# Kernel optimization log

Measured on AMD Instinct MI355X. Metric: run time of the kernel, lower is better.

The kernel has to match this reference:

```python
import jax, jax.numpy as jnp
import numpy as np

N_TOKENS = 4096
NUM_IN = 512
OUTPUT_DIMS = [512, 512, 256]
TOTAL_OUT = sum(OUTPUT_DIMS)  # 1280
N_EXPERTS = 8
TOP_K = 2
TEBD_DIM = 64
NTYPES = 128


def setup_inputs() -> dict:
    key = jax.random.key(0)
    ks = jax.random.split(key, 6)
    x = jax.random.normal(ks[0], (N_TOKENS, NUM_IN), dtype=jnp.float32)
    type_embeddings = jax.random.normal(ks[1], (NTYPES, TEBD_DIM), dtype=jnp.float32)
    atom_types = jax.random.randint(ks[2], (N_TOKENS,), 0, NTYPES)
    # learned parameters
    gate_in_dim = NUM_IN + TEBD_DIM
    W_gate = jax.random.normal(ks[3], (gate_in_dim, N_EXPERTS), dtype=jnp.float32) / np.sqrt(gate_in_dim)
    W_exp = jax.random.normal(ks[4], (N_EXPERTS, NUM_IN, TOTAL_OUT), dtype=jnp.float32) / np.sqrt(NUM_IN)
    b_exp = jax.random.normal(ks[5], (N_EXPERTS, TOTAL_OUT), dtype=jnp.float32) * 0.01
    return {"x": x, "type_embeddings": type_embeddings, "atom_types": atom_types,
            "W_gate": W_gate, "W_exp": W_exp, "b_exp": b_exp}


def reference(x, type_embeddings, atom_types, W_gate, W_exp, b_exp):
    # --- gating: atom-type-conditioned router (tebd_dim > 0) ---
    tebd = type_embeddings[atom_types]                      # [N, T]
    gate_in = jnp.concatenate([x, tebd], axis=-1)           # [N, D+T]
    logits = gate_in @ W_gate                               # [N, E]
    top_v, top_i = jax.lax.top_k(logits, TOP_K)             # [N, k]
    probs = jax.nn.softmax(top_v, axis=-1)                  # renormalized over selected experts
    # dense sparse-gate matrix [N, E] (zeros for unselected experts)
    gates = jnp.sum(jax.nn.one_hot(top_i, N_EXPERTS, dtype=x.dtype) * probs[..., None], axis=1)
    # --- expert compute (grouped GEMM expressed densely) ---
    y_all = jnp.einsum('nd,edo->neo', x, W_exp) + b_exp     # [N, E, O]
    fused = jnp.einsum('ne,neo->no', gates, y_all)          # [N, TOTAL_OUT]
    # --- split fused output per head ---
    splits = np.cumsum(OUTPUT_DIMS)[:-1].tolist()
    return tuple(jnp.split(fused, splits, axis=-1))
```

## Files before the change

kernel.cpp:

```cpp
#include <hip/hip_runtime.h>
#include <hip/hip_bf16.h>
#include <cstdint>
#include <cmath>

#define NT 4096
#define DIN 512
#define DOUT 1280
#define NE 8
#define TDIM 64
#define MAXTILES 80
#define NB 10
#define GATE_BLOCKS (NT / 4)
#define CONVW_BLOCKS (20 * (DIN / 64) * NE)
#define S1ROWS 5120

typedef __attribute__((ext_vector_type(8))) short bhalf8;
typedef __attribute__((ext_vector_type(8))) unsigned short ushort8;
typedef __attribute__((ext_vector_type(4))) float f32x4;

__device__ __forceinline__ unsigned short f2bf(float f) {
    __hip_bfloat16 h = __float2bfloat16(f);
    return *reinterpret_cast<unsigned short*>(&h);
}
__device__ __forceinline__ float bf2f(unsigned short u) {
    unsigned int v = (unsigned int)u << 16;
    return *reinterpret_cast<float*>(&v);
}

__device__ __forceinline__ void glds16(const unsigned short* g, unsigned short* l) {
    __builtin_amdgcn_global_load_lds(
        (const __attribute__((address_space(1))) void*)g,
        (__attribute__((address_space(3))) void*)l, 16, 0, 0);
}

__global__ __launch_bounds__(256) void prep_kernel(
    const float* __restrict__ x, const float* __restrict__ temb,
    const int* __restrict__ atype, const float* __restrict__ Wg,
    const float* __restrict__ W,
    unsigned short* __restrict__ xb, unsigned short* __restrict__ WT,
    int* __restrict__ e0a, int* __restrict__ e1a,
    float* __restrict__ g0a, float* __restrict__ g1a)
{
    __shared__ unsigned short t[64 * 72];
    const int tid = threadIdx.x;

    if ((int)blockIdx.x < GATE_BLOCKS) {
        const int n = blockIdx.x * 4 + (tid >> 6);
        const int l = tid & 63;

        float acc[NE];
#pragma unroll
        for (int e = 0; e < NE; ++e) acc[e] = 0.f;

        const float* xr = x + (size_t)n * DIN;
#pragma unroll
        for (int i = 0; i < DIN / 64; ++i) {
            const int k = i * 64 + l;
            const float xv = xr[k];
            xb[(size_t)n * DIN + k] = f2bf(xv);
            const float* wr = Wg + (size_t)k * NE;
#pragma unroll
            for (int e = 0; e < NE; ++e) acc[e] = fmaf(xv, wr[e], acc[e]);
        }
        {
            const int tt = atype[n];
            const float tv = temb[(size_t)tt * TDIM + l];
            const float* wr = Wg + (size_t)(DIN + l) * NE;
#pragma unroll
            for (int e = 0; e < NE; ++e) acc[e] = fmaf(tv, wr[e], acc[e]);
        }
#pragma unroll
        for (int off = 32; off > 0; off >>= 1) {
#pragma unroll
            for (int e = 0; e < NE; ++e) acc[e] += __shfl_xor(acc[e], off, 64);
        }
        if (l == 0) {
            int e0 = 0; float v0 = acc[0];
#pragma unroll
            for (int e = 1; e < NE; ++e) if (acc[e] > v0) { v0 = acc[e]; e0 = e; }
            int e1 = -1; float v1 = -INFINITY;
#pragma unroll
            for (int e = 0; e < NE; ++e) {
                if (e == e0) continue;
                if (acc[e] > v1) { v1 = acc[e]; e1 = e; }
            }
            const float p1 = expf(v1 - v0);
            const float s  = 1.f + p1;
            e0a[n] = e0; e1a[n] = e1; g0a[n] = 1.f / s; g1a[n] = p1 / s;
        }
    } else {
        const int b  = blockIdx.x - GATE_BLOCKS;
        const int n0 = (b % 20) * 64;
        const int k0 = ((b / 20) % (DIN / 64)) * 64;
        const int e  = b / (20 * (DIN / 64));
        const int nl = tid & 63;
        const int kb = tid >> 6;
#pragma unroll
        for (int r = 0; r < 16; ++r) {
            const int kl = r * 4 + kb;
            t[nl * 72 + kl] = f2bf(W[((size_t)e * DIN + k0 + kl) * DOUT + n0 + nl]);
        }
        __syncthreads();
        const int nw = tid >> 2;
        const int kc = tid & 3;
        uint4* dst = reinterpret_cast<uint4*>(
            WT + ((size_t)e * DOUT + n0 + nw) * DIN + k0 + kc * 16);
        const uint4* src = reinterpret_cast<const uint4*>(&t[nw * 72 + kc * 16]);
        dst[0] = src[0];
        dst[1] = src[1];
    }
}

#define SORT_T 1024
__global__ __launch_bounds__(1024) void sort_kernel(
    const int* __restrict__ e0a, const int* __restrict__ e1a,
    const float* __restrict__ g0a, const float* __restrict__ g1a,
    int* __restrict__ perm, float* __restrict__ pgate,
    int* __restrict__ tile_group, int* __restrict__ ipos1,
    int* __restrict__ meta2)
{
    __shared__ int hist[16 * SORT_T];
    __shared__ int gtot[16], gbase[16];
    const int t = threadIdx.x;
    for (int i = t; i < MAXTILES * 128; i += SORT_T) { perm[i] = 0; pgate[i] = 0.f; }
#pragma unroll
    for (int g = 0; g < 16; ++g) hist[g * SORT_T + t] = 0;
    __syncthreads();

    const int nbase = t * 4;
    int keys[8];
#pragma unroll
    for (int i = 0; i < 4; ++i) {
        const int n = nbase + i;
        keys[2 * i]     = e0a[n];
        keys[2 * i + 1] = 8 + e1a[n];
    }
#pragma unroll
    for (int i = 0; i < 8; ++i) hist[keys[i] * SORT_T + t] += 1;
    __syncthreads();

    const int w = t >> 6, l = t & 63;
    {
        int running = 0;
        for (int c = 0; c < SORT_T / 64; ++c) {
            int v = hist[w * SORT_T + c * 64 + l];
            int inc = v;
#pragma unroll
            for (int d = 1; d < 64; d <<= 1) {
                int u = __shfl_up(inc, d, 64);
                if (l >= d) inc += u;
            }
            hist[w * SORT_T + c * 64 + l] = running + inc - v;
            running += __shfl(inc, 63, 64);
        }
        if (l == 0) gtot[w] = running;
    }
    __syncthreads();
    if (t == 0) {
        int s = 0;
#pragma unroll
        for (int g = 0; g < 16; ++g) {
            gbase[g] = s;
            const int ntg = (gtot[g] + 127) >> 7;
            for (int k = 0; k < ntg; ++k) tile_group[s / 128 + k] = g;
            s += ntg * 128;
        }
        meta2[0] = s / 128;
        meta2[1] = gbase[8];
    }
    __syncthreads();

#pragma unroll
    for (int i = 0; i < 4; ++i) {
        const int n = nbase + i;
        {
            const int k = keys[2 * i];
            const int pos = gbase[k] + hist[k * SORT_T + t]++;
            perm[pos] = n; pgate[pos] = g0a[n];
        }
        {
            const int k = keys[2 * i + 1];
            const int pos = gbase[k] + hist[k * SORT_T + t]++;
            perm[pos] = n; pgate[pos] = g1a[n];
            ipos1[n] = pos - gbase[8];
        }
    }
}

__device__ __forceinline__ int swz(int row, int chunk) {
    return row * 64 + ((chunk ^ (row & 7)) << 3);
}

__global__ __launch_bounds__(256, 4) void gemm_kernel(
    const unsigned short* __restrict__ Xb,
    const unsigned short* __restrict__ WT,
    const float* __restrict__ bexp,
    const int* __restrict__ perm, const float* __restrict__ pgate,
    const int* __restrict__ tile_group, const int* __restrict__ meta2,
    unsigned short* __restrict__ stage, float* __restrict__ out)
{
    constexpr int NWG = MAXTILES * NB, CPX = NWG / 8;
    const int gid = blockIdx.x;
    const int wid = (gid & 7) * CPX + (gid >> 3);
    const int tile = wid / NB, nb = wid % NB;
    if (tile >= meta2[0]) return;
    const int g  = tile_group[tile];
    const int e  = g & 7;
    const bool s1 = (g >= 8);
    const int n0 = nb * 128;
    const int ph = tile & 7;

    __shared__ unsigned short As[128 * 64];
    __shared__ unsigned short Bs[128 * 64];
    __shared__ int   toks[128];
    __shared__ float gts[128];

    const int tid = threadIdx.x;
    if (tid < 128) {
        toks[tid] = perm[tile * 128 + tid];
        gts[tid]  = pgate[tile * 128 + tid];
    }
    __syncthreads();

    const int l = tid & 63;
    const int w = tid >> 6;
    const int lrow = l >> 3;
    const int schk = (l & 7) ^ lrow;

    const unsigned short* asrc[4];
    unsigned short* aldsb[4];
#pragma unroll
    for (int i = 0; i < 4; ++i) {
        asrc[i]  = Xb + (size_t)toks[i * 32 + w * 8 + lrow] * DIN + schk * 8;
        aldsb[i] = &As[(i * 32 + w * 8) * 64];
    }
    const unsigned short* bsrc[4];
    unsigned short* bldsb[4];
#pragma unroll
    for (int j = 0; j < 4; ++j) {
        bsrc[j]  = WT + ((size_t)e * DOUT + n0 + j * 32 + w * 8 + lrow) * DIN + schk * 8;
        bldsb[j] = &Bs[(j * 32 + w * 8) * 64];
    }

    f32x4 acc[4][4];
#pragma unroll
    for (int a = 0; a < 4; ++a)
#pragma unroll
        for (int b = 0; b < 4; ++b) acc[a][b] = (f32x4){0.f, 0.f, 0.f, 0.f};

    const int wm = w >> 1, wn = w & 1;
    const int fr = l & 15;
    const int fh = l >> 4;

#pragma unroll
    for (int t = 0; t < DIN / 64; ++t) {
        const int k0 = (((t + ph) & 7)) * 64;
        __syncthreads();
#pragma unroll
        for (int i = 0; i < 4; ++i) glds16(asrc[i] + k0, aldsb[i]);
#pragma unroll
        for (int j = 0; j < 4; ++j) glds16(bsrc[j] + k0, bldsb[j]);
        __syncthreads();
#pragma unroll
        for (int ks = 0; ks < 2; ++ks) {
            bhalf8 af[4], bff[4];
#pragma unroll
            for (int fm = 0; fm < 4; ++fm)
                af[fm] = *reinterpret_cast<const bhalf8*>(
                    &As[swz(wm * 64 + fm * 16 + fr, ks * 4 + fh)]);
#pragma unroll
            for (int fn = 0; fn < 4; ++fn)
                bff[fn] = *reinterpret_cast<const bhalf8*>(
                    &Bs[swz(wn * 64 + fn * 16 + fr, ks * 4 + fh)]);
#pragma unroll
            for (int fm = 0; fm < 4; ++fm)
#pragma unroll
                for (int fn = 0; fn < 4; ++fn)
                    acc[fm][fn] = __builtin_amdgcn_mfma_f32_16x16x32_bf16(
                        af[fm], bff[fn], acc[fm][fn], 0, 0, 0);
        }
    }

    const int lc = l & 15, lr = l >> 4;
    float bval[4];
#pragma unroll
    for (int fn = 0; fn < 4; ++fn)
        bval[fn] = bexp[(size_t)e * DOUT + n0 + wn * 64 + fn * 16 + lc];

    if (s1) {
        const int srow0 = tile * 128 - meta2[1];
#pragma unroll
        for (int fm = 0; fm < 4; ++fm) {
#pragma unroll
            for (int j = 0; j < 4; ++j) {
                const int row = wm * 64 + fm * 16 + lr * 4 + j;
                const float gg = gts[row];
                unsigned short* sp = stage + (size_t)(srow0 + row) * DOUT + n0 + wn * 64 + lc;
#pragma unroll
                for (int fn = 0; fn < 4; ++fn)
                    sp[fn * 16] = f2bf(gg * (acc[fm][fn][j] + bval[fn]));
            }
        }
    } else {
        size_t base; int width, cstart;
        if (n0 < 512)       { base = 0;                 width = 512; cstart = n0; }
        else if (n0 < 1024) { base = (size_t)NT * 512;  width = 512; cstart = n0 - 512; }
        else                { base = (size_t)NT * 1024; width = 256; cstart = n0 - 1024; }
        const int coloff = cstart + wn * 64 + lc;
#pragma unroll
        for (int fm = 0; fm < 4; ++fm) {
#pragma unroll
            for (int j = 0; j < 4; ++j) {
                const int row = wm * 64 + fm * 16 + lr * 4 + j;
                const float gg = gts[row];
                if (gg != 0.f) {
                    float* op = out + base + (size_t)toks[row] * width + coloff;
#pragma unroll
                    for (int fn = 0; fn < 4; ++fn)
                        op[fn * 16] = gg * (acc[fm][fn][j] + bval[fn]);
                }
            }
        }
    }
}

__global__ __launch_bounds__(256) void combine_kernel(
    const unsigned short* __restrict__ stage, const int* __restrict__ ipos1,
    float* __restrict__ out)
{
    const int n = blockIdx.x * 4 + (threadIdx.x >> 6);
    const int l = threadIdx.x & 63;
    const ushort8* srow = reinterpret_cast<const ushort8*>(
        stage + (size_t)ipos1[n] * DOUT);
#pragma unroll
    for (int c = l; c < DOUT / 8; c += 64) {
        const ushort8 v8 = srow[c];
        const int col0 = c * 8;
        float* p;
        if (col0 < 512)       p = out + (size_t)n * 512 + col0;
        else if (col0 < 1024) p = out + (size_t)NT * 512 + (size_t)n * 512 + (col0 - 512);
        else                  p = out + (size_t)NT * 1024 + (size_t)n * 256 + (col0 - 1024);
        f32x4* pv = reinterpret_cast<f32x4*>(p);
        f32x4 a0 = pv[0], a1 = pv[1];
#pragma unroll
        for (int j = 0; j < 4; ++j) a0[j] += bf2f(v8[j]);
#pragma unroll
        for (int j = 0; j < 4; ++j) a1[j] += bf2f(v8[4 + j]);
        pv[0] = a0; pv[1] = a1;
    }
}

extern "C" void kernel_launch(void* const* d_in, const int* in_sizes, int n_in,
                              void* d_out, int out_size, void* d_ws, size_t ws_size,
                              hipStream_t stream) {
    const float* x     = (const float*)d_in[0];
    const float* temb  = (const float*)d_in[1];
    const int*   atype = (const int*)d_in[2];
    const float* Wg    = (const float*)d_in[3];
    const float* Wexp  = (const float*)d_in[4];
    const float* bexp  = (const float*)d_in[5];
    float* out = (float*)d_out;
    char*  ws  = (char*)d_ws;

    unsigned short* xb = (unsigned short*)(ws);
    unsigned short* wt = (unsigned short*)(ws + (size_t)4194304);
    unsigned short* stage = (unsigned short*)(ws + (size_t)14680064);
    const size_t META = 14680064 + (size_t)S1ROWS * DOUT * 2;
    char* meta = ws + META;
    int*   e0a = (int*)(meta);
    int*   e1a = (int*)(meta + 16384);
    float* g0a = (float*)(meta + 32768);
    float* g1a = (float*)(meta + 49152);
    int*   perm       = (int*)(meta + 65536);
    float* pgate      = (float*)(meta + 106496);
    int*   tile_group = (int*)(meta + 147456);
    int*   ipos1      = (int*)(meta + 147968);
    int*   meta2      = (int*)(meta + 164352);

    prep_kernel<<<dim3(GATE_BLOCKS + CONVW_BLOCKS), dim3(256), 0, stream>>>(
        x, temb, atype, Wg, Wexp, xb, wt, e0a, e1a, g0a, g1a);
    sort_kernel<<<dim3(1), dim3(SORT_T), 0, stream>>>(
        e0a, e1a, g0a, g1a, perm, pgate, tile_group, ipos1, meta2);
    gemm_kernel<<<dim3(MAXTILES * NB), dim3(256), 0, stream>>>(
        xb, wt, bexp, perm, pgate, tile_group, meta2, stage, out);
    combine_kernel<<<dim3(NT / 4), dim3(256), 0, stream>>>(stage, ipos1, out);
}
```

Before: 61.40 us.

## Overlap routing sort with weight conversion; vectorize gate x loads

The weight bf16 transpose-conversion moves out of the gating kernel and into a new kernel whose block 0 does the expert sort (now 256 threads, 16 tokens each), while the other 1280 blocks convert weights. The single-block sort therefore overlaps the weight conversion instead of running alone serially. The gating kernel now loads x as 8 contiguous floats per lane and writes bf16 as one 16-byte store. Risks: block 0 has a long serial sort that may become the tail of the mixed kernel, and the smaller sort block has less parallelism.

```diff
diff --git a/kernel.cpp b/kernel.cpp
--- a/kernel.cpp
+++ b/kernel.cpp
@@ -10,8 +10,6 @@
 #define TDIM 64
 #define MAXTILES 80
 #define NB 10
-#define GATE_BLOCKS (NT / 4)
-#define CONVW_BLOCKS (20 * (DIN / 64) * NE)
 #define S1ROWS 5120
 
 typedef __attribute__((ext_vector_type(8))) short bhalf8;
@@ -33,157 +31,158 @@
         (__attribute__((address_space(3))) void*)l, 16, 0, 0);
 }
 
-__global__ __launch_bounds__(256) void prep_kernel(
+__global__ __launch_bounds__(256) void gate_kernel(
     const float* __restrict__ x, const float* __restrict__ temb,
     const int* __restrict__ atype, const float* __restrict__ Wg,
-    const float* __restrict__ W,
-    unsigned short* __restrict__ xb, unsigned short* __restrict__ WT,
+    unsigned short* __restrict__ xb,
     int* __restrict__ e0a, int* __restrict__ e1a,
     float* __restrict__ g0a, float* __restrict__ g1a)
 {
-    __shared__ unsigned short t[64 * 72];
-    const int tid = threadIdx.x;
-
-    if ((int)blockIdx.x < GATE_BLOCKS) {
-        const int n = blockIdx.x * 4 + (tid >> 6);
-        const int l = tid & 63;
-
-        float acc[NE];
-#pragma unroll
-        for (int e = 0; e < NE; ++e) acc[e] = 0.f;
-
-        const float* xr = x + (size_t)n * DIN;
-#pragma unroll
-        for (int i = 0; i < DIN / 64; ++i) {
-            const int k = i * 64 + l;
-            const float xv = xr[k];
-            xb[(size_t)n * DIN + k] = f2bf(xv);
-            const float* wr = Wg + (size_t)k * NE;
-#pragma unroll
-            for (int e = 0; e < NE; ++e) acc[e] = fmaf(xv, wr[e], acc[e]);
-        }
-        {
-            const int tt = atype[n];
-            const float tv = temb[(size_t)tt * TDIM + l];
-            const float* wr = Wg + (size_t)(DIN + l) * NE;
-#pragma unroll
-            for (int e = 0; e < NE; ++e) acc[e] = fmaf(tv, wr[e], acc[e]);
-        }
-#pragma unroll
-        for (int off = 32; off > 0; off >>= 1) {
-#pragma unroll
-            for (int e = 0; e < NE; ++e) acc[e] += __shfl_xor(acc[e], off, 64);
-        }
-        if (l == 0) {
-            int e0 = 0; float v0 = acc[0];
-#pragma unroll
-            for (int e = 1; e < NE; ++e) if (acc[e] > v0) { v0 = acc[e]; e0 = e; }
-            int e1 = -1; float v1 = -INFINITY;
-#pragma unroll
-            for (int e = 0; e < NE; ++e) {
-                if (e == e0) continue;
-                if (acc[e] > v1) { v1 = acc[e]; e1 = e; }
-            }
-            const float p1 = expf(v1 - v0);
-            const float s  = 1.f + p1;
-            e0a[n] = e0; e1a[n] = e1; g0a[n] = 1.f / s; g1a[n] = p1 / s;
-        }
-    } else {
-        const int b  = blockIdx.x - GATE_BLOCKS;
-        const int n0 = (b % 20) * 64;
-        const int k0 = ((b / 20) % (DIN / 64)) * 64;
-        const int e  = b / (20 * (DIN / 64));
-        const int nl = tid & 63;
-        const int kb = tid >> 6;
-#pragma unroll
-        for (int r = 0; r < 16; ++r) {
-            const int kl = r * 4 + kb;
-            t[nl * 72 + kl] = f2bf(W[((size_t)e * DIN + k0 + kl) * DOUT + n0 + nl]);
-        }
-        __syncthreads();
-        const int nw = tid >> 2;
-        const int kc = tid & 3;
-        uint4* dst = reinterpret_cast<uint4*>(
-            WT + ((size_t)e * DOUT + n0 + nw) * DIN + k0 + kc * 16);
-        const uint4* src = reinterpret_cast<const uint4*>(&t[nw * 72 + kc * 16]);
-        dst[0] = src[0];
-        dst[1] = src[1];
-    }
-}
-
-#define SORT_T 1024
-__global__ __launch_bounds__(1024) void sort_kernel(
+    const int n = blockIdx.x * 4 + (threadIdx.x >> 6);
+    const int l = threadIdx.x & 63;
+
+    float acc[NE];
+#pragma unroll
+    for (int e = 0; e < NE; ++e) acc[e] = 0.f;
+
+    const f32x4* xr = reinterpret_cast<const f32x4*>(x + (size_t)n * DIN);
+    const f32x4 v0 = xr[l * 2], v1 = xr[l * 2 + 1];
+    float xv[8] = {v0[0], v0[1], v0[2], v0[3], v1[0], v1[1], v1[2], v1[3]};
+    ushort8 xo;
+#pragma unroll
+    for (int j = 0; j < 8; ++j) xo[j] = f2bf(xv[j]);
+    *reinterpret_cast<ushort8*>(xb + (size_t)n * DIN + l * 8) = xo;
+#pragma unroll
+    for (int j = 0; j < 8; ++j) {
+        const float* wr = Wg + (size_t)(l * 8 + j) * NE;
+#pragma unroll
+        for (int e = 0; e < NE; ++e) acc[e] = fmaf(xv[j], wr[e], acc[e]);
+    }
+    {
+        const int tt = atype[n];
+        const float tv = temb[(size_t)tt * TDIM + l];
+        const float* wr = Wg + (size_t)(DIN + l) * NE;
+#pragma unroll
+        for (int e = 0; e < NE; ++e) acc[e] = fmaf(tv, wr[e], acc[e]);
+    }
+#pragma unroll
+    for (int off = 32; off > 0; off >>= 1) {
+#pragma unroll
+        for (int e = 0; e < NE; ++e) acc[e] += __shfl_xor(acc[e], off, 64);
+    }
+    if (l == 0) {
+        int e0 = 0; float v = acc[0];
+#pragma unroll
+        for (int e = 1; e < NE; ++e) if (acc[e] > v) { v = acc[e]; e0 = e; }
+        int e1 = -1; float v1m = -INFINITY;
+#pragma unroll
+        for (int e = 0; e < NE; ++e) {
+            if (e == e0) continue;
+            if (acc[e] > v1m) { v1m = acc[e]; e1 = e; }
+        }
+        const float p1 = expf(v1m - v);
+        const float s  = 1.f + p1;
+        e0a[n] = e0; e1a[n] = e1; g0a[n] = 1.f / s; g1a[n] = p1 / s;
+    }
+}
+
+#define ST 256
+__global__ __launch_bounds__(256) void mix_kernel(
+    const float* __restrict__ W, unsigned short* __restrict__ WT,
     const int* __restrict__ e0a, const int* __restrict__ e1a,
     const float* __restrict__ g0a, const float* __restrict__ g1a,
     int* __restrict__ perm, float* __restrict__ pgate,
     int* __restrict__ tile_group, int* __restrict__ ipos1,
     int* __restrict__ meta2)
 {
-    __shared__ int hist[16 * SORT_T];
+    __shared__ int hist[16 * ST];
     __shared__ int gtot[16], gbase[16];
+    __shared__ unsigned short tbuf[64 * 72];
     const int t = threadIdx.x;
-    for (int i = t; i < MAXTILES * 128; i += SORT_T) { perm[i] = 0; pgate[i] = 0.f; }
-#pragma unroll
-    for (int g = 0; g < 16; ++g) hist[g * SORT_T + t] = 0;
-    __syncthreads();
-
-    const int nbase = t * 4;
-    int keys[8];
-#pragma unroll
-    for (int i = 0; i < 4; ++i) {
-        const int n = nbase + i;
-        keys[2 * i]     = e0a[n];
-        keys[2 * i + 1] = 8 + e1a[n];
-    }
-#pragma unroll
-    for (int i = 0; i < 8; ++i) hist[keys[i] * SORT_T + t] += 1;
-    __syncthreads();
-
-    const int w = t >> 6, l = t & 63;
-    {
-        int running = 0;
-        for (int c = 0; c < SORT_T / 64; ++c) {
-            int v = hist[w * SORT_T + c * 64 + l];
-            int inc = v;
-#pragma unroll
-            for (int d = 1; d < 64; d <<= 1) {
-                int u = __shfl_up(inc, d, 64);
-                if (l >= d) inc += u;
-            }
-            hist[w * SORT_T + c * 64 + l] = running + inc - v;
-            running += __shfl(inc, 63, 64);
-        }
-        if (l == 0) gtot[w] = running;
-    }
-    __syncthreads();
-    if (t == 0) {
-        int s = 0;
-#pragma unroll
-        for (int g = 0; g < 16; ++g) {
-            gbase[g] = s;
-            const int ntg = (gtot[g] + 127) >> 7;
-            for (int k = 0; k < ntg; ++k) tile_group[s / 128 + k] = g;
-            s += ntg * 128;
-        }
-        meta2[0] = s / 128;
-        meta2[1] = gbase[8];
-    }
-    __syncthreads();
-
-#pragma unroll
-    for (int i = 0; i < 4; ++i) {
-        const int n = nbase + i;
-        {
-            const int k = keys[2 * i];
-            const int pos = gbase[k] + hist[k * SORT_T + t]++;
-            perm[pos] = n; pgate[pos] = g0a[n];
-        }
-        {
-            const int k = keys[2 * i + 1];
-            const int pos = gbase[k] + hist[k * SORT_T + t]++;
-            perm[pos] = n; pgate[pos] = g1a[n];
-            ipos1[n] = pos - gbase[8];
-        }
+
+    if (blockIdx.x == 0) {
+        for (int i = t; i < MAXTILES * 128; i += ST) { perm[i] = 0; pgate[i] = 0.f; }
+#pragma unroll
+        for (int g = 0; g < 16; ++g) hist[g * ST + t] = 0;
+        __syncthreads();
+
+#pragma unroll
+        for (int i = 0; i < 16; ++i) {
+            const int n = t * 16 + i;
+            hist[e0a[n] * ST + t] += 1;
+            hist[(8 + e1a[n]) * ST + t] += 1;
+        }
+        __syncthreads();
+
+        const int w = t >> 6, l = t & 63;
+#pragma unroll
+        for (int q = 0; q < 4; ++q) {
+            const int g = w * 4 + q;
+            int running = 0;
+#pragma unroll
+            for (int c = 0; c < ST / 64; ++c) {
+                int v = hist[g * ST + c * 64 + l];
+                int inc = v;
+#pragma unroll
+                for (int d = 1; d < 64; d <<= 1) {
+                    int u = __shfl_up(inc, d, 64);
+                    if (l >= d) inc += u;
+                }
+                hist[g * ST + c * 64 + l] = running + inc - v;
+                running += __shfl(inc, 63, 64);
+            }
+            if (l == 0) gtot[g] = running;
+        }
+        __syncthreads();
+        if (t == 0) {
+            int s = 0;
+#pragma unroll
+            for (int g = 0; g < 16; ++g) {
+                gbase[g] = s;
+                const int ntg = (gtot[g] + 127) >> 7;
+                for (int k = 0; k < ntg; ++k) tile_group[s / 128 + k] = g;
+                s += ntg * 128;
+            }
+            meta2[0] = s / 128;
+            meta2[1] = gbase[8];
+        }
+        __syncthreads();
+
+#pragma unroll
+        for (int i = 0; i < 16; ++i) {
+            const int n = t * 16 + i;
+            {
+                const int k = e0a[n];
+                const int pos = gbase[k] + hist[k * ST + t]++;
+                perm[pos] = n; pgate[pos] = g0a[n];
+            }
+            {
+                const int k = 8 + e1a[n];
+                const int pos = gbase[k] + hist[k * ST + t]++;
+                perm[pos] = n; pgate[pos] = g1a[n];
+                ipos1[n] = pos - gbase[8];
+            }
+        }
+    } else {
+        const int b  = blockIdx.x - 1;
+        const int n0 = (b % 20) * 64;
+        const int k0 = ((b / 20) % (DIN / 64)) * 64;
+        const int e  = b / (20 * (DIN / 64));
+        const int nl = t & 63;
+        const int kb = t >> 6;
+#pragma unroll
+        for (int r = 0; r < 16; ++r) {
+            const int kl = r * 4 + kb;
+            tbuf[nl * 72 + kl] = f2bf(W[((size_t)e * DIN + k0 + kl) * DOUT + n0 + nl]);
+        }
+        __syncthreads();
+        const int nw = t >> 2;
+        const int kc = t & 3;
+        uint4* dst = reinterpret_cast<uint4*>(
+            WT + ((size_t)e * DOUT + n0 + nw) * DIN + k0 + kc * 16);
+        const uint4* src = reinterpret_cast<const uint4*>(&tbuf[nw * 72 + kc * 16]);
+        dst[0] = src[0];
+        dst[1] = src[1];
     }
 }
 
@@ -254,7 +253,7 @@
 
 #pragma unroll
     for (int t = 0; t < DIN / 64; ++t) {
-        const int k0 = (((t + ph) & 7)) * 64;
+        const int k0 = ((t + ph) & 7) * 64;
         __syncthreads();
 #pragma unroll
         for (int i = 0; i < 4; ++i) glds16(asrc[i] + k0, aldsb[i]);
@@ -377,10 +376,10 @@
     int*   ipos1      = (int*)(meta + 147968);
     int*   meta2      = (int*)(meta + 164352);
 
-    prep_kernel<<<dim3(GATE_BLOCKS + CONVW_BLOCKS), dim3(256), 0, stream>>>(
-        x, temb, atype, Wg, Wexp, xb, wt, e0a, e1a, g0a, g1a);
-    sort_kernel<<<dim3(1), dim3(SORT_T), 0, stream>>>(
-        e0a, e1a, g0a, g1a, perm, pgate, tile_group, ipos1, meta2);
+    gate_kernel<<<dim3(NT / 4), dim3(256), 0, stream>>>(
+        x, temb, atype, Wg, xb, e0a, e1a, g0a, g1a);
+    mix_kernel<<<dim3(1 + 1280), dim3(256), 0, stream>>>(
+        Wexp, wt, e0a, e1a, g0a, g1a, perm, pgate, tile_group, ipos1, meta2);
     gemm_kernel<<<dim3(MAXTILES * NB), dim3(256), 0, stream>>>(
         xb, wt, bexp, perm, pgate, tile_group, meta2, stage, out);
     combine_kernel<<<dim3(NT / 4), dim3(256), 0, stream>>>(stage, ipos1, out);
```

Measured after the change: 67.05 us. 1.09x slower.
